# Kernel tuning notes

Hardware: AMD Instinct MI355X
Metric: run time of the kernel (lower is better)

## Reference

```python
import jax, jax.numpy as jnp
import numpy as np

N = 10000       # nodes
E = 640000      # edges (avg degree 64)
F_IN = 128      # num_node_features
H = 128         # hid_size
C = 16          # num_classes


def setup_inputs() -> dict:
    key = jax.random.key(0)
    ks = jax.random.split(key, 12)
    g = lambda k, shape, fan: jax.random.normal(k, shape, jnp.float32) * (1.0 / np.sqrt(fan))
    return {
        "x": jax.random.normal(ks[0], (N, F_IN), jnp.float32),
        "edge_index": jax.random.randint(ks[1], (2, E), 0, N, dtype=jnp.int32),
        "W1": g(ks[2], (F_IN, H), F_IN), "b1": jnp.zeros((H,), jnp.float32),
        "W2": g(ks[3], (H, H), H),       "b2": jnp.zeros((H,), jnp.float32),
        "Wlin1": g(ks[4], (H, C), H),    "blin1": jnp.zeros((C,), jnp.float32),
        "Wdeg2": g(ks[5], (H, 1), H),    "bdeg2": jnp.zeros((1,), jnp.float32),
        "Wdeg3": g(ks[6], (H, 1), H),    "bdeg3": jnp.zeros((1,), jnp.float32),
        "Wdown": g(ks[7], (F_IN, H), F_IN), "bdown": jnp.zeros((H,), jnp.float32),
    }


def _gcn_norm(edge_index):
    # PyG GCNConv: add self-loops, symmetric normalization d^-1/2 A d^-1/2
    loops = jnp.arange(N, dtype=edge_index.dtype)
    src = jnp.concatenate([edge_index[0], loops])   # [E+N]
    dst = jnp.concatenate([edge_index[1], loops])   # [E+N]
    deg = jax.ops.segment_sum(jnp.ones_like(dst, jnp.float32), dst, num_segments=N)
    dis = jnp.where(deg > 0, jax.lax.rsqrt(jnp.maximum(deg, 1.0)), 0.0)
    norm = dis[src] * dis[dst]                      # [E+N]
    return src, dst, norm


def _gcn_conv(h, W, b, src, dst, norm):
    h = h @ W                                       # [N, H] transform first (smaller dim)
    msg = h[src] * norm[:, None]                    # gather + edge weight
    return jax.ops.segment_sum(msg, dst, num_segments=N) + b


def reference(x, edge_index, W1, b1, W2, b2, Wlin1, blin1, Wdeg2, bdeg2, Wdeg3, bdeg3, Wdown, bdown):
    src, dst, norm = _gcn_norm(edge_index)
    original = x @ Wdown + bdown                    # down_sample residual
    h = jax.nn.relu(_gcn_conv(x, W1, b1, src, dst, norm))
    # dropout is identity in eval mode
    h = _gcn_conv(h, W2, b2, src, dst, norm) + original
    result1 = jax.nn.log_softmax(h @ Wlin1 + blin1, axis=1)   # [N, C]
    result2 = (h @ Wdeg2 + bdeg2)[:, 0]                        # [N]
    result3 = (h @ Wdeg3 + bdeg3)[:, 0]                        # [N]
    return (result1, result2, result3)
```

## Files before the change

### kernel.cpp

```cpp
#include <hip/hip_runtime.h>
#include <math.h>

#define N_NODES 10000
#define N_EDGES 640000
#define NB      100
#define CH      (N_EDGES / NB)
#define HP      10016
#define GB      313
#define NBLK    40
#define NPB2    250

typedef unsigned short ushort4_t __attribute__((ext_vector_type(4)));
typedef unsigned short ushort8_t __attribute__((ext_vector_type(8)));

__device__ inline unsigned short f2bf(float f) {
    unsigned int u = __float_as_uint(f);
    u = (u + 0x7FFFu + ((u >> 16) & 1u)) >> 16;
    return (unsigned short)u;
}
__device__ inline float bf2f(unsigned short s) {
    return __uint_as_float(((unsigned int)s) << 16);
}

__device__ __forceinline__ void gbar(int* bar, int slot, int nblk) {
    __syncthreads();
    if (threadIdx.x == 0) {
        int* cnt = bar + slot;
        int* gen = bar + 8 + slot;
        int g = atomicAdd(gen, 0);
        __threadfence();
        if (atomicAdd(cnt, 1) == nblk - 1) {
            __threadfence();
            atomicAdd(gen, 1);
        } else {
            while (atomicAdd(gen, 0) == g) __builtin_amdgcn_s_sleep(4);
        }
        __threadfence();
    }
    __syncthreads();
}

__global__ __launch_bounds__(256) void k_hist_gemm2(const int* __restrict__ dst,
                                                    int* __restrict__ hmat,
                                                    unsigned short* __restrict__ rank,
                                                    int* __restrict__ bar,
                                                    const float* __restrict__ X,
                                                    const float* __restrict__ W1,
                                                    const float* __restrict__ Wdown,
                                                    const float* __restrict__ bdown,
                                                    unsigned short* __restrict__ outT,
                                                    float* __restrict__ outB, int n) {
    __shared__ char smem[81920];
    int t = threadIdx.x;

    if (blockIdx.x < NB) {
        int* hs = (int*)smem;
        if (blockIdx.x == 0 && t < 16) bar[t] = 0;
        for (int j = t; j < HP; j += 256) hs[j] = 0;
        __syncthreads();
        int base = blockIdx.x * CH;
#pragma unroll 4
        for (int j = t; j < CH; j += 256) {
            int r = atomicAdd(&hs[dst[base + j]], 1);
            rank[base + j] = (unsigned short)r;
        }
        __syncthreads();
        int* out = hmat + blockIdx.x * HP;
        for (int j = t; j < N_NODES; j += 256) out[j] = hs[j];
        return;
    }

    float* xs = (float*)smem;
    float* wsm = (float*)(smem + 16384);
    int bid = blockIdx.x - NB;
    int which = (bid >= GB) ? 1 : 0;
    int bx = which ? bid - GB : bid;
    int tile0 = bx * 32;
    const float* W = which ? Wdown : W1;

    const float4* Wv = (const float4*)W;
    float4* wsv = (float4*)wsm;
#pragma unroll
    for (int q = 0; q < 16; ++q) wsv[t + 256 * q] = Wv[t + 256 * q];

    const float4* Xv = (const float4*)X;
    float4* xsv = (float4*)xs;
#pragma unroll
    for (int q = 0; q < 4; ++q) {
        int idx = t + 256 * q;
        int row = tile0 + (idx >> 5);
        float4 v = make_float4(0.f, 0.f, 0.f, 0.f);
        if (row < n) v = Xv[(size_t)row * 32 + (idx & 31)];
        xsv[idx] = v;
    }
    __syncthreads();

    int c4 = t & 31;
    int rg = t >> 5;
    float4 acc[4];
#pragma unroll
    for (int p = 0; p < 4; ++p) acc[p] = make_float4(0.f, 0.f, 0.f, 0.f);

    const float4* wsr = (const float4*)wsm;
    const float4* xsr = (const float4*)xs;
#pragma unroll 4
    for (int kq = 0; kq < 32; ++kq) {
        float4 w0 = wsr[(4 * kq + 0) * 32 + c4];
        float4 w1 = wsr[(4 * kq + 1) * 32 + c4];
        float4 w2 = wsr[(4 * kq + 2) * 32 + c4];
        float4 w3 = wsr[(4 * kq + 3) * 32 + c4];
#pragma unroll
        for (int p = 0; p < 4; ++p) {
            float4 xv = xsr[(rg * 4 + p) * 32 + kq];
            acc[p].x += xv.x * w0.x + xv.y * w1.x + xv.z * w2.x + xv.w * w3.x;
            acc[p].y += xv.x * w0.y + xv.y * w1.y + xv.z * w2.y + xv.w * w3.y;
            acc[p].z += xv.x * w0.z + xv.y * w1.z + xv.z * w2.z + xv.w * w3.z;
            acc[p].w += xv.x * w0.w + xv.y * w1.w + xv.z * w2.w + xv.w * w3.w;
        }
    }
    if (which == 0) {
#pragma unroll
        for (int p = 0; p < 4; ++p) {
            int row = tile0 + rg * 4 + p;
            if (row < n) {
                ushort4_t o;
                o[0] = f2bf(acc[p].x); o[1] = f2bf(acc[p].y);
                o[2] = f2bf(acc[p].z); o[3] = f2bf(acc[p].w);
                ((ushort4_t*)outT)[(size_t)row * 32 + c4] = o;
            }
        }
    } else {
        float4 bv = ((const float4*)bdown)[c4];
#pragma unroll
        for (int p = 0; p < 4; ++p) {
            int row = tile0 + rg * 4 + p;
            if (row < n) {
                float4 o;
                o.x = acc[p].x + bv.x; o.y = acc[p].y + bv.y;
                o.z = acc[p].z + bv.z; o.w = acc[p].w + bv.w;
                ((float4*)outB)[(size_t)row * 32 + c4] = o;
            }
        }
    }
}

__global__ __launch_bounds__(256) void k_mid(const int* __restrict__ h,
                                             int* bar,
                                             int* __restrict__ rangesum,
                                             int* __restrict__ offsets,
                                             float* __restrict__ dis,
                                             int* __restrict__ bmat) {
    __shared__ int sc[256];
    __shared__ int rsl[NBLK];
    __shared__ int sP;
    int b = blockIdx.x, t = threadIdx.x;
    int i = b * NPB2 + t;
    bool act = (t < NPB2);

    int s = 0;
    if (act) {
#pragma unroll 5
        for (int bb = 0; bb < NB; ++bb) s += h[bb * HP + i];
        dis[i] = rsqrtf((float)(s + 1));
    }
    sc[t] = s;
    __syncthreads();
#pragma unroll
    for (int off = 1; off < 256; off <<= 1) {
        int v = (t >= off) ? sc[t - off] : 0;
        __syncthreads();
        sc[t] += v;
        __syncthreads();
    }
    int lofs = sc[t] - s;
    if (t == 255) rangesum[b] = sc[255];
    gbar(bar, 0, NBLK);

    if (t < NBLK) rsl[t] = rangesum[t];
    __syncthreads();
    if (t == 0) {
        int P = 0;
        for (int bb = 0; bb < b; ++bb) P += rsl[bb];
        sP = P;
        if (b == NBLK - 1) offsets[N_NODES] = P + rsl[b];
    }
    __syncthreads();
    if (act) {
        int run = sP + lofs;
        offsets[i] = run;
#pragma unroll 5
        for (int bb = 0; bb < NB; ++bb) {
            bmat[bb * HP + i] = run;
            run += h[bb * HP + i];
        }
    }
}

__global__ __launch_bounds__(256) void k_scatter_ep(const int* __restrict__ src,
                                                    const int* __restrict__ dst,
                                                    const unsigned short* __restrict__ rank,
                                                    const int* __restrict__ bmat,
                                                    int* __restrict__ csr) {
    int e = blockIdx.x * 256 + threadIdx.x;
    int b = blockIdx.x / (CH / 256);
    int d = dst[e];
    int s = src[e];
    int r = rank[e];
    int pos = bmat[b * HP + d] + r;
    csr[pos] = s;
}

__global__ __launch_bounds__(256) void k_gemm(const float* __restrict__ X,
                                              const float* __restrict__ W,
                                              unsigned short* __restrict__ Y, int n) {
    __shared__ float xs[32 * 128];
    __shared__ float ws[128 * 128];
    int t = threadIdx.x;
    int tile0 = blockIdx.x * 32;

    const float4* Wv = (const float4*)W;
    float4* wsv = (float4*)ws;
#pragma unroll
    for (int q = 0; q < 16; ++q) wsv[t + 256 * q] = Wv[t + 256 * q];

    const float4* Xv = (const float4*)X;
    float4* xsv = (float4*)xs;
#pragma unroll
    for (int q = 0; q < 4; ++q) {
        int idx = t + 256 * q;
        int row = tile0 + (idx >> 5);
        float4 v = make_float4(0.f, 0.f, 0.f, 0.f);
        if (row < n) v = Xv[(size_t)row * 32 + (idx & 31)];
        xsv[idx] = v;
    }
    __syncthreads();

    int c4 = t & 31;
    int rg = t >> 5;
    float4 acc[4];
#pragma unroll
    for (int p = 0; p < 4; ++p) acc[p] = make_float4(0.f, 0.f, 0.f, 0.f);

    const float4* wsr = (const float4*)ws;
    const float4* xsr = (const float4*)xs;
#pragma unroll 4
    for (int kq = 0; kq < 32; ++kq) {
        float4 w0 = wsr[(4 * kq + 0) * 32 + c4];
        float4 w1 = wsr[(4 * kq + 1) * 32 + c4];
        float4 w2 = wsr[(4 * kq + 2) * 32 + c4];
        float4 w3 = wsr[(4 * kq + 3) * 32 + c4];
#pragma unroll
        for (int p = 0; p < 4; ++p) {
            float4 xv = xsr[(rg * 4 + p) * 32 + kq];
            acc[p].x += xv.x * w0.x + xv.y * w1.x + xv.z * w2.x + xv.w * w3.x;
            acc[p].y += xv.x * w0.y + xv.y * w1.y + xv.z * w2.y + xv.w * w3.y;
            acc[p].z += xv.x * w0.z + xv.y * w1.z + xv.z * w2.z + xv.w * w3.z;
            acc[p].w += xv.x * w0.w + xv.y * w1.w + xv.z * w2.w + xv.w * w3.w;
        }
    }
#pragma unroll
    for (int p = 0; p < 4; ++p) {
        int row = tile0 + rg * 4 + p;
        if (row < n) {
            ushort4_t o;
            o[0] = f2bf(acc[p].x); o[1] = f2bf(acc[p].y);
            o[2] = f2bf(acc[p].z); o[3] = f2bf(acc[p].w);
            ((ushort4_t*)Y)[(size_t)row * 32 + c4] = o;
        }
    }
}

__global__ __launch_bounds__(256) void k_agg1(const unsigned short* __restrict__ T,
                                              const float* __restrict__ dis,
                                              const int* __restrict__ offsets,
                                              const int* __restrict__ csr,
                                              const float* __restrict__ bias,
                                              float* __restrict__ Y, int n) {
    __shared__ float red[3][16][9];
    int i = blockIdx.x;
    int t = threadIdx.x;
    int c8 = t & 15;
    int es = t >> 4;
    int wave = t >> 6;
    int lane = t & 63;

    int e0 = offsets[i], e1 = offsets[i + 1];
    const ushort8_t* T8 = (const ushort8_t*)T;

    float acc[8];
#pragma unroll
    for (int j = 0; j < 8; ++j) acc[j] = 0.f;

    int e = e0 + es;
    for (; e + 16 < e1; e += 32) {
        int s0 = csr[e];
        int s1 = csr[e + 16];
        float w0 = dis[s0];
        float w1 = dis[s1];
        ushort8_t v0 = T8[(size_t)s0 * 16 + c8];
        ushort8_t v1 = T8[(size_t)s1 * 16 + c8];
#pragma unroll
        for (int j = 0; j < 8; ++j)
            acc[j] += w0 * bf2f(v0[j]) + w1 * bf2f(v1[j]);
    }
    if (e < e1) {
        int s0 = csr[e];
        float w0 = dis[s0];
        ushort8_t v0 = T8[(size_t)s0 * 16 + c8];
#pragma unroll
        for (int j = 0; j < 8; ++j) acc[j] += w0 * bf2f(v0[j]);
    }

#pragma unroll
    for (int j = 0; j < 8; ++j) {
        acc[j] += __shfl_xor(acc[j], 16, 64);
        acc[j] += __shfl_xor(acc[j], 32, 64);
    }
    if (wave > 0 && lane < 16) {
#pragma unroll
        for (int j = 0; j < 8; ++j) red[wave - 1][lane][j] = acc[j];
    }
    __syncthreads();
    if (wave == 0 && lane < 16) {
#pragma unroll
        for (int j = 0; j < 8; ++j)
            acc[j] += red[0][lane][j] + red[1][lane][j] + red[2][lane][j];

        float di = dis[i];
        ushort8_t sv = T8[(size_t)i * 16 + c8];
#pragma unroll
        for (int j = 0; j < 8; ++j) acc[j] += di * bf2f(sv[j]);
#pragma unroll
        for (int j = 0; j < 8; ++j)
            acc[j] = fmaxf(di * acc[j] + bias[c8 * 8 + j], 0.f);

        float4* Y4 = (float4*)Y;
        Y4[(size_t)i * 32 + c8 * 2]     = make_float4(acc[0], acc[1], acc[2], acc[3]);
        Y4[(size_t)i * 32 + c8 * 2 + 1] = make_float4(acc[4], acc[5], acc[6], acc[7]);
    }
}

__global__ __launch_bounds__(256) void k_agg2h(const unsigned short* __restrict__ T,
                                               const float* __restrict__ dis,
                                               const int* __restrict__ offsets,
                                               const int* __restrict__ csr,
                                               const float* __restrict__ bias,
                                               const float* __restrict__ resid,
                                               const float* __restrict__ Wlin,
                                               const float* __restrict__ blin,
                                               const float* __restrict__ Wd2,
                                               const float* __restrict__ bd2,
                                               const float* __restrict__ Wd3,
                                               const float* __restrict__ bd3,
                                               float* __restrict__ out1,
                                               float* __restrict__ out2,
                                               float* __restrict__ out3, int n) {
    __shared__ float red[3][16][9];
    __shared__ float hrow[128];
    int i = blockIdx.x;
    int t = threadIdx.x;
    int c8 = t & 15;
    int es = t >> 4;
    int wave = t >> 6;
    int lane = t & 63;

    int e0 = offsets[i], e1 = offsets[i + 1];
    const ushort8_t* T8 = (const ushort8_t*)T;

    float acc[8];
#pragma unroll
    for (int j = 0; j < 8; ++j) acc[j] = 0.f;

    int e = e0 + es;
    for (; e + 16 < e1; e += 32) {
        int s0 = csr[e];
        int s1 = csr[e + 16];
        float w0 = dis[s0];
        float w1 = dis[s1];
        ushort8_t v0 = T8[(size_t)s0 * 16 + c8];
        ushort8_t v1 = T8[(size_t)s1 * 16 + c8];
#pragma unroll
        for (int j = 0; j < 8; ++j)
            acc[j] += w0 * bf2f(v0[j]) + w1 * bf2f(v1[j]);
    }
    if (e < e1) {
        int s0 = csr[e];
        float w0 = dis[s0];
        ushort8_t v0 = T8[(size_t)s0 * 16 + c8];
#pragma unroll
        for (int j = 0; j < 8; ++j) acc[j] += w0 * bf2f(v0[j]);
    }

#pragma unroll
    for (int j = 0; j < 8; ++j) {
        acc[j] += __shfl_xor(acc[j], 16, 64);
        acc[j] += __shfl_xor(acc[j], 32, 64);
    }
    if (wave > 0 && lane < 16) {
#pragma unroll
        for (int j = 0; j < 8; ++j) red[wave - 1][lane][j] = acc[j];
    }
    __syncthreads();
    if (wave == 0 && lane < 16) {
#pragma unroll
        for (int j = 0; j < 8; ++j)
            acc[j] += red[0][lane][j] + red[1][lane][j] + red[2][lane][j];

        float di = dis[i];
        ushort8_t sv = T8[(size_t)i * 16 + c8];
#pragma unroll
        for (int j = 0; j < 8; ++j) acc[j] += di * bf2f(sv[j]);

        const float4* rv4 = (const float4*)resid;
        float4 r0 = rv4[(size_t)i * 32 + c8 * 2];
        float4 r1 = rv4[(size_t)i * 32 + c8 * 2 + 1];
#pragma unroll
        for (int j = 0; j < 8; ++j) acc[j] = di * acc[j] + bias[c8 * 8 + j];
        acc[0] += r0.x; acc[1] += r0.y; acc[2] += r0.z; acc[3] += r0.w;
        acc[4] += r1.x; acc[5] += r1.y; acc[6] += r1.z; acc[7] += r1.w;

#pragma unroll
        for (int j = 0; j < 8; ++j) hrow[c8 * 8 + j] = acc[j];
    }
    __syncthreads();

    if (wave == 0) {
        float h0 = hrow[lane];
        float h1 = hrow[64 + lane];
        float p2 = h0 * Wd2[lane] + h1 * Wd2[64 + lane];
        float p3 = h0 * Wd3[lane] + h1 * Wd3[64 + lane];
#pragma unroll
        for (int d = 1; d < 64; d <<= 1) {
            p2 += __shfl_xor(p2, d, 64);
            p3 += __shfl_xor(p3, d, 64);
        }
        if (lane == 0) {
            out2[i] = p2 + bd2[0];
            out3[i] = p3 + bd3[0];
        }
        int c = lane & 15, kg = lane >> 4;
        float z = 0.f;
#pragma unroll 8
        for (int j = 0; j < 32; ++j) {
            int k = kg * 32 + j;
            z += hrow[k] * Wlin[k * 16 + c];
        }
        z += __shfl_xor(z, 16, 64);
        z += __shfl_xor(z, 32, 64);
        z += blin[c];
        float m = z;
#pragma unroll
        for (int d = 1; d < 16; d <<= 1) m = fmaxf(m, __shfl_xor(m, d, 64));
        float ex = expf(z - m);
        float ssum = ex;
#pragma unroll
        for (int d = 1; d < 16; d <<= 1) ssum += __shfl_xor(ssum, d, 64);
        float lsm = z - m - logf(ssum);
        if (lane < 16) out1[(size_t)i * 16 + c] = lsm;
    }
}

extern "C" void kernel_launch(void* const* d_in, const int* in_sizes, int n_in,
                              void* d_out, int out_size, void* d_ws, size_t ws_size,
                              hipStream_t stream) {
    const float* x     = (const float*)d_in[0];
    const int*   ei    = (const int*)d_in[1];
    const float* W1    = (const float*)d_in[2];
    const float* b1    = (const float*)d_in[3];
    const float* W2    = (const float*)d_in[4];
    const float* b2    = (const float*)d_in[5];
    const float* Wlin1 = (const float*)d_in[6];
    const float* blin1 = (const float*)d_in[7];
    const float* Wdeg2 = (const float*)d_in[8];
    const float* bdeg2 = (const float*)d_in[9];
    const float* Wdeg3 = (const float*)d_in[10];
    const float* bdeg3 = (const float*)d_in[11];
    const float* Wdown = (const float*)d_in[12];
    const float* bdown = (const float*)d_in[13];

    const int n = N_NODES, E = N_EDGES;
    const int* src = ei;
    const int* dst = ei + E;

    char* ws = (char*)d_ws;
    int*            bar      = (int*)ws;
    int*            hmat     = bar + 64;
    int*            bmat     = hmat + NB * HP;
    int*            rangesum = bmat + NB * HP;
    int*            offsets  = rangesum + 64;
    float*          dis      = (float*)(offsets + 10048);
    unsigned short* rank     = (unsigned short*)(dis + HP);
    int*            csr      = (int*)(rank + E);
    unsigned short* bufT     = (unsigned short*)(csr + E);
    float*          bufB     = (float*)(bufT + (size_t)n * 128);
    float*          bufC     = bufB + (size_t)n * 128;

    k_hist_gemm2<<<NB + 2 * GB, 256, 0, stream>>>(dst, hmat, rank, bar, x, W1,
                                                  Wdown, bdown, bufT, bufB, n);
    k_mid<<<NBLK, 256, 0, stream>>>(hmat, bar, rangesum, offsets, dis, bmat);
    k_scatter_ep<<<E / 256, 256, 0, stream>>>(src, dst, rank, bmat, csr);
    k_agg1<<<n, 256, 0, stream>>>(bufT, dis, offsets, csr, b1, bufC, n);
    k_gemm<<<(n + 31) / 32, 256, 0, stream>>>(bufC, W2, bufT, n);
    float* out1 = (float*)d_out;
    float* out2 = out1 + (size_t)n * 16;
    float* out3 = out2 + n;
    k_agg2h<<<n, 256, 0, stream>>>(bufT, dis, offsets, csr, b2, bufB,
                                   Wlin1, blin1, Wdeg2, bdeg2, Wdeg3, bdeg3,
                                   out1, out2, out3, n);
}
```

Measured before the change: 105.0 us.

## Fuse CSR scatter into scan kernel, store dis with edges, one wave per node

Merges the offset scan and the edge scatter into one persistent kernel with 256 blocks and two grid barriers, removing one launch. The scatter now writes (src, dis[src]) pairs so the aggregation kernels skip the dependent dis gather. Both aggregation kernels now map one wave per node instead of one block per node, which removes the shared-memory reduction and __syncthreads, and they unroll four edges per iteration. The head computation is redone with in-wave shuffles. The trade-offs are a larger edge record buffer to read and write, and a grid-barrier kernel whose 256 blocks must all be co-resident.

```diff
diff --git a/kernel.cpp b/kernel.cpp
--- a/kernel.cpp
+++ b/kernel.cpp
@@ -7,8 +7,10 @@
 #define CH      (N_EDGES / NB)
 #define HP      10016
 #define GB      313
-#define NBLK    40
+#define NMID    40
 #define NPB2    250
+#define SCB     256
+#define EPB     (N_EDGES / SCB)
 
 typedef unsigned short ushort4_t __attribute__((ext_vector_type(4)));
 typedef unsigned short ushort8_t __attribute__((ext_vector_type(8)));
@@ -144,70 +146,78 @@
     }
 }
 
-__global__ __launch_bounds__(256) void k_mid(const int* __restrict__ h,
-                                             int* bar,
-                                             int* __restrict__ rangesum,
-                                             int* __restrict__ offsets,
-                                             float* __restrict__ dis,
-                                             int* __restrict__ bmat) {
+__global__ __launch_bounds__(256) void k_midsc(const int* __restrict__ src,
+                                               const int* __restrict__ dst,
+                                               const unsigned short* __restrict__ rank,
+                                               const int* __restrict__ h,
+                                               int* bar,
+                                               int* __restrict__ rangesum,
+                                               int* __restrict__ offsets,
+                                               float* __restrict__ dis,
+                                               int* __restrict__ bmat,
+                                               int2* __restrict__ rec) {
     __shared__ int sc[256];
-    __shared__ int rsl[NBLK];
+    __shared__ int rsl[NMID];
     __shared__ int sP;
     int b = blockIdx.x, t = threadIdx.x;
     int i = b * NPB2 + t;
-    bool act = (t < NPB2);
-
-    int s = 0;
-    if (act) {
-#pragma unroll 5
-        for (int bb = 0; bb < NB; ++bb) s += h[bb * HP + i];
-        dis[i] = rsqrtf((float)(s + 1));
-    }
-    sc[t] = s;
-    __syncthreads();
-#pragma unroll
-    for (int off = 1; off < 256; off <<= 1) {
-        int v = (t >= off) ? sc[t - off] : 0;
+    bool mid = (b < NMID);
+    bool act = mid && (t < NPB2);
+    int s = 0, lofs = 0;
+
+    if (mid) {
+        if (act) {
+#pragma unroll 10
+            for (int bb = 0; bb < NB; ++bb) s += h[bb * HP + i];
+            dis[i] = rsqrtf((float)(s + 1));
+        }
+        sc[t] = s;
         __syncthreads();
-        sc[t] += v;
+#pragma unroll
+        for (int off = 1; off < 256; off <<= 1) {
+            int v = (t >= off) ? sc[t - off] : 0;
+            __syncthreads();
+            sc[t] += v;
+            __syncthreads();
+        }
+        lofs = sc[t] - s;
+        if (t == 255) rangesum[b] = sc[255];
+    }
+    gbar(bar, 0, SCB);
+
+    if (mid) {
+        if (t < NMID) rsl[t] = rangesum[t];
         __syncthreads();
-    }
-    int lofs = sc[t] - s;
-    if (t == 255) rangesum[b] = sc[255];
-    gbar(bar, 0, NBLK);
-
-    if (t < NBLK) rsl[t] = rangesum[t];
-    __syncthreads();
-    if (t == 0) {
-        int P = 0;
-        for (int bb = 0; bb < b; ++bb) P += rsl[bb];
-        sP = P;
-        if (b == NBLK - 1) offsets[N_NODES] = P + rsl[b];
-    }
-    __syncthreads();
-    if (act) {
-        int run = sP + lofs;
-        offsets[i] = run;
-#pragma unroll 5
-        for (int bb = 0; bb < NB; ++bb) {
-            bmat[bb * HP + i] = run;
-            run += h[bb * HP + i];
-        }
-    }
-}
-
-__global__ __launch_bounds__(256) void k_scatter_ep(const int* __restrict__ src,
-                                                    const int* __restrict__ dst,
-                                                    const unsigned short* __restrict__ rank,
-                                                    const int* __restrict__ bmat,
-                                                    int* __restrict__ csr) {
-    int e = blockIdx.x * 256 + threadIdx.x;
-    int b = blockIdx.x / (CH / 256);
-    int d = dst[e];
-    int s = src[e];
-    int r = rank[e];
-    int pos = bmat[b * HP + d] + r;
-    csr[pos] = s;
+        if (t == 0) {
+            int P = 0;
+            for (int bb = 0; bb < b; ++bb) P += rsl[bb];
+            sP = P;
+            if (b == NMID - 1) offsets[N_NODES] = P + rsl[b];
+        }
+        __syncthreads();
+        if (act) {
+            int run = sP + lofs;
+            offsets[i] = run;
+#pragma unroll 10
+            for (int bb = 0; bb < NB; ++bb) {
+                bmat[bb * HP + i] = run;
+                run += h[bb * HP + i];
+            }
+        }
+    }
+    gbar(bar, 1, SCB);
+
+    int base = b * EPB;
+#pragma unroll 4
+    for (int j = t; j < EPB; j += 256) {
+        int e = base + j;
+        int d = dst[e];
+        int sv = src[e];
+        int r = rank[e];
+        int chunk = e / CH;
+        int pos = bmat[chunk * HP + d] + r;
+        rec[pos] = make_int2(sv, __float_as_int(dis[sv]));
+    }
 }
 
 __global__ __launch_bounds__(256) void k_gemm(const float* __restrict__ X,
@@ -270,193 +280,140 @@
     }
 }
 
-__global__ __launch_bounds__(256) void k_agg1(const unsigned short* __restrict__ T,
-                                              const float* __restrict__ dis,
-                                              const int* __restrict__ offsets,
-                                              const int* __restrict__ csr,
-                                              const float* __restrict__ bias,
-                                              float* __restrict__ Y, int n) {
-    __shared__ float red[3][16][9];
-    int i = blockIdx.x;
-    int t = threadIdx.x;
-    int c8 = t & 15;
-    int es = t >> 4;
-    int wave = t >> 6;
-    int lane = t & 63;
-
+#define AGG_EDGE_LOOP                                                          \
+    float acc[8];                                                              \
+    _Pragma("unroll") for (int j = 0; j < 8; ++j) acc[j] = 0.f;                \
+    int e = e0 + es;                                                           \
+    for (; e + 12 < e1; e += 16) {                                             \
+        int2 r0 = rec[e], r1 = rec[e + 4], r2 = rec[e + 8], r3 = rec[e + 12];  \
+        float w0 = __int_as_float(r0.y), w1 = __int_as_float(r1.y);            \
+        float w2 = __int_as_float(r2.y), w3 = __int_as_float(r3.y);            \
+        ushort8_t v0 = T8[(size_t)r0.x * 16 + c8];                             \
+        ushort8_t v1 = T8[(size_t)r1.x * 16 + c8];                             \
+        ushort8_t v2 = T8[(size_t)r2.x * 16 + c8];                             \
+        ushort8_t v3 = T8[(size_t)r3.x * 16 + c8];                             \
+        _Pragma("unroll") for (int j = 0; j < 8; ++j)                          \
+            acc[j] += w0 * bf2f(v0[j]) + w1 * bf2f(v1[j]) +                    \
+                      w2 * bf2f(v2[j]) + w3 * bf2f(v3[j]);                     \
+    }                                                                          \
+    for (; e < e1; e += 4) {                                                   \
+        int2 r0 = rec[e];                                                      \
+        float w0 = __int_as_float(r0.y);                                       \
+        ushort8_t v0 = T8[(size_t)r0.x * 16 + c8];                             \
+        _Pragma("unroll") for (int j = 0; j < 8; ++j)                          \
+            acc[j] += w0 * bf2f(v0[j]);                                        \
+    }                                                                          \
+    _Pragma("unroll") for (int j = 0; j < 8; ++j) {                            \
+        acc[j] += __shfl_xor(acc[j], 16, 64);                                  \
+        acc[j] += __shfl_xor(acc[j], 32, 64);                                  \
+    }
+
+__global__ __launch_bounds__(256) void k_agg1w(const ushort8_t* __restrict__ T8,
+                                               const float* __restrict__ dis,
+                                               const int* __restrict__ offsets,
+                                               const int2* __restrict__ rec,
+                                               const float* __restrict__ bias,
+                                               float* __restrict__ Y) {
+    int wave = threadIdx.x >> 6, lane = threadIdx.x & 63;
+    int i = blockIdx.x * 4 + wave;
+    int c8 = lane & 15, es = lane >> 4;
     int e0 = offsets[i], e1 = offsets[i + 1];
-    const ushort8_t* T8 = (const ushort8_t*)T;
-
-    float acc[8];
-#pragma unroll
-    for (int j = 0; j < 8; ++j) acc[j] = 0.f;
-
-    int e = e0 + es;
-    for (; e + 16 < e1; e += 32) {
-        int s0 = csr[e];
-        int s1 = csr[e + 16];
-        float w0 = dis[s0];
-        float w1 = dis[s1];
-        ushort8_t v0 = T8[(size_t)s0 * 16 + c8];
-        ushort8_t v1 = T8[(size_t)s1 * 16 + c8];
-#pragma unroll
-        for (int j = 0; j < 8; ++j)
-            acc[j] += w0 * bf2f(v0[j]) + w1 * bf2f(v1[j]);
-    }
-    if (e < e1) {
-        int s0 = csr[e];
-        float w0 = dis[s0];
-        ushort8_t v0 = T8[(size_t)s0 * 16 + c8];
-#pragma unroll
-        for (int j = 0; j < 8; ++j) acc[j] += w0 * bf2f(v0[j]);
-    }
-
-#pragma unroll
-    for (int j = 0; j < 8; ++j) {
-        acc[j] += __shfl_xor(acc[j], 16, 64);
-        acc[j] += __shfl_xor(acc[j], 32, 64);
-    }
-    if (wave > 0 && lane < 16) {
-#pragma unroll
-        for (int j = 0; j < 8; ++j) red[wave - 1][lane][j] = acc[j];
-    }
-    __syncthreads();
-    if (wave == 0 && lane < 16) {
-#pragma unroll
-        for (int j = 0; j < 8; ++j)
-            acc[j] += red[0][lane][j] + red[1][lane][j] + red[2][lane][j];
-
-        float di = dis[i];
-        ushort8_t sv = T8[(size_t)i * 16 + c8];
-#pragma unroll
-        for (int j = 0; j < 8; ++j) acc[j] += di * bf2f(sv[j]);
-#pragma unroll
-        for (int j = 0; j < 8; ++j)
-            acc[j] = fmaxf(di * acc[j] + bias[c8 * 8 + j], 0.f);
-
+
+    AGG_EDGE_LOOP
+
+    float di = dis[i];
+    ushort8_t sv = T8[(size_t)i * 16 + c8];
+#pragma unroll
+    for (int j = 0; j < 8; ++j) acc[j] += di * bf2f(sv[j]);
+#pragma unroll
+    for (int j = 0; j < 8; ++j)
+        acc[j] = fmaxf(di * acc[j] + bias[c8 * 8 + j], 0.f);
+
+    if (es == 0) {
         float4* Y4 = (float4*)Y;
         Y4[(size_t)i * 32 + c8 * 2]     = make_float4(acc[0], acc[1], acc[2], acc[3]);
         Y4[(size_t)i * 32 + c8 * 2 + 1] = make_float4(acc[4], acc[5], acc[6], acc[7]);
     }
 }
 
-__global__ __launch_bounds__(256) void k_agg2h(const unsigned short* __restrict__ T,
-                                               const float* __restrict__ dis,
-                                               const int* __restrict__ offsets,
-                                               const int* __restrict__ csr,
-                                               const float* __restrict__ bias,
-                                               const float* __restrict__ resid,
-                                               const float* __restrict__ Wlin,
-                                               const float* __restrict__ blin,
-                                               const float* __restrict__ Wd2,
-                                               const float* __restrict__ bd2,
-                                               const float* __restrict__ Wd3,
-                                               const float* __restrict__ bd3,
-                                               float* __restrict__ out1,
-                                               float* __restrict__ out2,
-                                               float* __restrict__ out3, int n) {
-    __shared__ float red[3][16][9];
-    __shared__ float hrow[128];
-    int i = blockIdx.x;
-    int t = threadIdx.x;
-    int c8 = t & 15;
-    int es = t >> 4;
-    int wave = t >> 6;
-    int lane = t & 63;
-
+__global__ __launch_bounds__(256) void k_agg2hw(const ushort8_t* __restrict__ T8,
+                                                const float* __restrict__ dis,
+                                                const int* __restrict__ offsets,
+                                                const int2* __restrict__ rec,
+                                                const float* __restrict__ bias,
+                                                const float* __restrict__ resid,
+                                                const float* __restrict__ Wlin,
+                                                const float* __restrict__ blin,
+                                                const float* __restrict__ Wd2,
+                                                const float* __restrict__ bd2,
+                                                const float* __restrict__ Wd3,
+                                                const float* __restrict__ bd3,
+                                                float* __restrict__ out1,
+                                                float* __restrict__ out2,
+                                                float* __restrict__ out3) {
+    int wave = threadIdx.x >> 6, lane = threadIdx.x & 63;
+    int i = blockIdx.x * 4 + wave;
+    int c8 = lane & 15, es = lane >> 4;
     int e0 = offsets[i], e1 = offsets[i + 1];
-    const ushort8_t* T8 = (const ushort8_t*)T;
-
-    float acc[8];
-#pragma unroll
-    for (int j = 0; j < 8; ++j) acc[j] = 0.f;
-
-    int e = e0 + es;
-    for (; e + 16 < e1; e += 32) {
-        int s0 = csr[e];
-        int s1 = csr[e + 16];
-        float w0 = dis[s0];
-        float w1 = dis[s1];
-        ushort8_t v0 = T8[(size_t)s0 * 16 + c8];
-        ushort8_t v1 = T8[(size_t)s1 * 16 + c8];
+
+    AGG_EDGE_LOOP
+
+    float di = dis[i];
+    ushort8_t sv = T8[(size_t)i * 16 + c8];
+#pragma unroll
+    for (int j = 0; j < 8; ++j) acc[j] += di * bf2f(sv[j]);
+#pragma unroll
+    for (int j = 0; j < 8; ++j) acc[j] = di * acc[j] + bias[c8 * 8 + j];
+    const float4* rv4 = (const float4*)resid;
+    float4 r0 = rv4[(size_t)i * 32 + c8 * 2];
+    float4 r1 = rv4[(size_t)i * 32 + c8 * 2 + 1];
+    acc[0] += r0.x; acc[1] += r0.y; acc[2] += r0.z; acc[3] += r0.w;
+    acc[4] += r1.x; acc[5] += r1.y; acc[6] += r1.z; acc[7] += r1.w;
+
+    float p2 = 0.f, p3 = 0.f;
+#pragma unroll
+    for (int j = 0; j < 8; ++j) {
+        p2 += acc[j] * Wd2[c8 * 8 + j];
+        p3 += acc[j] * Wd3[c8 * 8 + j];
+    }
+#pragma unroll
+    for (int d = 1; d < 16; d <<= 1) {
+        p2 += __shfl_xor(p2, d, 64);
+        p3 += __shfl_xor(p3, d, 64);
+    }
+    if (lane == 0) {
+        out2[i] = p2 + bd2[0];
+        out3[i] = p3 + bd3[0];
+    }
+
+    float pc[4];
+#pragma unroll
+    for (int q = 0; q < 4; ++q) {
+        float z = 0.f;
 #pragma unroll
         for (int j = 0; j < 8; ++j)
-            acc[j] += w0 * bf2f(v0[j]) + w1 * bf2f(v1[j]);
-    }
-    if (e < e1) {
-        int s0 = csr[e];
-        float w0 = dis[s0];
-        ushort8_t v0 = T8[(size_t)s0 * 16 + c8];
-#pragma unroll
-        for (int j = 0; j < 8; ++j) acc[j] += w0 * bf2f(v0[j]);
-    }
-
-#pragma unroll
-    for (int j = 0; j < 8; ++j) {
-        acc[j] += __shfl_xor(acc[j], 16, 64);
-        acc[j] += __shfl_xor(acc[j], 32, 64);
-    }
-    if (wave > 0 && lane < 16) {
-#pragma unroll
-        for (int j = 0; j < 8; ++j) red[wave - 1][lane][j] = acc[j];
-    }
-    __syncthreads();
-    if (wave == 0 && lane < 16) {
-#pragma unroll
-        for (int j = 0; j < 8; ++j)
-            acc[j] += red[0][lane][j] + red[1][lane][j] + red[2][lane][j];
-
-        float di = dis[i];
-        ushort8_t sv = T8[(size_t)i * 16 + c8];
-#pragma unroll
-        for (int j = 0; j < 8; ++j) acc[j] += di * bf2f(sv[j]);
-
-        const float4* rv4 = (const float4*)resid;
-        float4 r0 = rv4[(size_t)i * 32 + c8 * 2];
-        float4 r1 = rv4[(size_t)i * 32 + c8 * 2 + 1];
-#pragma unroll
-        for (int j = 0; j < 8; ++j) acc[j] = di * acc[j] + bias[c8 * 8 + j];
-        acc[0] += r0.x; acc[1] += r0.y; acc[2] += r0.z; acc[3] += r0.w;
-        acc[4] += r1.x; acc[5] += r1.y; acc[6] += r1.z; acc[7] += r1.w;
-
-#pragma unroll
-        for (int j = 0; j < 8; ++j) hrow[c8 * 8 + j] = acc[j];
-    }
-    __syncthreads();
-
-    if (wave == 0) {
-        float h0 = hrow[lane];
-        float h1 = hrow[64 + lane];
-        float p2 = h0 * Wd2[lane] + h1 * Wd2[64 + lane];
-        float p3 = h0 * Wd3[lane] + h1 * Wd3[64 + lane];
-#pragma unroll
-        for (int d = 1; d < 64; d <<= 1) {
-            p2 += __shfl_xor(p2, d, 64);
-            p3 += __shfl_xor(p3, d, 64);
-        }
-        if (lane == 0) {
-            out2[i] = p2 + bd2[0];
-            out3[i] = p3 + bd3[0];
-        }
-        int c = lane & 15, kg = lane >> 4;
-        float z = 0.f;
-#pragma unroll 8
-        for (int j = 0; j < 32; ++j) {
-            int k = kg * 32 + j;
-            z += hrow[k] * Wlin[k * 16 + c];
-        }
-        z += __shfl_xor(z, 16, 64);
-        z += __shfl_xor(z, 32, 64);
-        z += blin[c];
-        float m = z;
-#pragma unroll
-        for (int d = 1; d < 16; d <<= 1) m = fmaxf(m, __shfl_xor(m, d, 64));
-        float ex = expf(z - m);
-        float ssum = ex;
-#pragma unroll
-        for (int d = 1; d < 16; d <<= 1) ssum += __shfl_xor(ssum, d, 64);
-        float lsm = z - m - logf(ssum);
-        if (lane < 16) out1[(size_t)i * 16 + c] = lsm;
+            z += acc[j] * Wlin[(c8 * 8 + j) * 16 + es * 4 + q];
+        pc[q] = z;
+    }
+#pragma unroll
+    for (int d = 1; d < 16; d <<= 1) {
+#pragma unroll
+        for (int q = 0; q < 4; ++q) pc[q] += __shfl_xor(pc[q], d, 64);
+    }
+#pragma unroll
+    for (int q = 0; q < 4; ++q) pc[q] += blin[es * 4 + q];
+
+    float m = fmaxf(fmaxf(pc[0], pc[1]), fmaxf(pc[2], pc[3]));
+    m = fmaxf(m, __shfl_xor(m, 16, 64));
+    m = fmaxf(m, __shfl_xor(m, 32, 64));
+    float ss = expf(pc[0] - m) + expf(pc[1] - m) + expf(pc[2] - m) + expf(pc[3] - m);
+    ss += __shfl_xor(ss, 16, 64);
+    ss += __shfl_xor(ss, 32, 64);
+    float lg = logf(ss);
+    if (c8 == 0) {
+#pragma unroll
+        for (int q = 0; q < 4; ++q)
+            out1[(size_t)i * 16 + es * 4 + q] = pc[q] - m - lg;
     }
 }
 
@@ -490,21 +447,23 @@
     int*            offsets  = rangesum + 64;
     float*          dis      = (float*)(offsets + 10048);
     unsigned short* rank     = (unsigned short*)(dis + HP);
-    int*            csr      = (int*)(rank + E);
-    unsigned short* bufT     = (unsigned short*)(csr + E);
+    int2*           rec      = (int2*)(rank + E);
+    unsigned short* bufT     = (unsigned short*)(rec + E);
     float*          bufB     = (float*)(bufT + (size_t)n * 128);
     float*          bufC     = bufB + (size_t)n * 128;
 
     k_hist_gemm2<<<NB + 2 * GB, 256, 0, stream>>>(dst, hmat, rank, bar, x, W1,
                                                   Wdown, bdown, bufT, bufB, n);
-    k_mid<<<NBLK, 256, 0, stream>>>(hmat, bar, rangesum, offsets, dis, bmat);
-    k_scatter_ep<<<E / 256, 256, 0, stream>>>(src, dst, rank, bmat, csr);
-    k_agg1<<<n, 256, 0, stream>>>(bufT, dis, offsets, csr, b1, bufC, n);
+    k_midsc<<<SCB, 256, 0, stream>>>(src, dst, rank, hmat, bar, rangesum,
+                                     offsets, dis, bmat, rec);
+    k_agg1w<<<n / 4, 256, 0, stream>>>((const ushort8_t*)bufT, dis, offsets,
+                                       rec, b1, bufC);
     k_gemm<<<(n + 31) / 32, 256, 0, stream>>>(bufC, W2, bufT, n);
     float* out1 = (float*)d_out;
     float* out2 = out1 + (size_t)n * 16;
     float* out3 = out2 + n;
-    k_agg2h<<<n, 256, 0, stream>>>(bufT, dis, offsets, csr, b2, bufB,
-                                   Wlin1, blin1, Wdeg2, bdeg2, Wdeg3, bdeg3,
-                                   out1, out2, out3, n);
-}
+    k_agg2hw<<<n / 4, 256, 0, stream>>>((const ushort8_t*)bufT, dis, offsets,
+                                        rec, b2, bufB, Wlin1, blin1,
+                                        Wdeg2, bdeg2, Wdeg3, bdeg3,
+                                        out1, out2, out3);
+}
```

Result: slower. 130.0 us (+23.8%).
